# Kernel tuning notes

Measured on AMD Instinct MI355X. Metric: run time of the kernel, lower is better.

Reference implementation:

```python
import jax, jax.numpy as jnp
import numpy as np

N_NODES = 50000
N_EDGES = 312500
WIDTH = 256
LN_EPS = 1e-5


def setup_inputs() -> dict:
    key = jax.random.key(0)
    k1, k2, k3, k4 = jax.random.split(key, 4)
    x = jax.random.normal(k1, (N_NODES, WIDTH), dtype=jnp.float32)
    edge_index = jax.random.randint(k2, (2, N_EDGES), 0, N_NODES, dtype=jnp.int64)
    # GCNConv linear weight (out, in) and bias, LayerNorm affine params
    W = jax.random.normal(k3, (WIDTH, WIDTH), dtype=jnp.float32) / np.sqrt(WIDTH)
    b = jax.random.normal(k4, (WIDTH,), dtype=jnp.float32) * 0.01
    gamma = jnp.ones((WIDTH,), dtype=jnp.float32)
    beta = jnp.zeros((WIDTH,), dtype=jnp.float32)
    return {"x": x, "edge_index": edge_index, "W": W, "b": b, "gamma": gamma, "beta": beta}


def gcn_conv(x, edge_index, W, b):
    """PyG GCNConv: add self-loops, symmetric normalization, scatter-add aggregate."""
    n = x.shape[0]
    loops = jnp.arange(n, dtype=edge_index.dtype)
    src = jnp.concatenate([edge_index[0], loops])  # message source
    dst = jnp.concatenate([edge_index[1], loops])  # message destination
    # degree computed on destination nodes (including self-loops)
    deg = jax.ops.segment_sum(jnp.ones_like(dst, dtype=x.dtype), dst, num_segments=n)
    dinv = jnp.where(deg > 0, jax.lax.rsqrt(deg), 0.0)
    norm = dinv[src] * dinv[dst]  # [E+N]
    h = x @ W.T  # [N, width]
    msgs = norm[:, None] * h[src]  # [E+N, width]
    out = jax.ops.segment_sum(msgs, dst, num_segments=n)
    return out + b


def layer_norm(x, gamma, beta):
    mu = jnp.mean(x, axis=-1, keepdims=True)
    var = jnp.mean(jnp.square(x - mu), axis=-1, keepdims=True)
    return (x - mu) * jax.lax.rsqrt(var + LN_EPS) * gamma + beta


def reference(x, edge_index, W, b, gamma, beta):
    h = gcn_conv(x, edge_index, W, b)
    h = layer_norm(h, gamma, beta)
    h = jax.nn.relu(h)
    # dropout is identity in eval mode
    return h
```

## Files before the change

### kernel.cpp

```cpp
#include <hip/hip_runtime.h>
#include <hip/hip_bf16.h>

#define N_NODES 50000
#define N_EDGES 312500
#define WIDTH   256
#define LN_EPS  1e-5f
#define CAP     64

typedef __attribute__((ext_vector_type(8))) short bf16x8;
typedef __attribute__((ext_vector_type(4))) float f32x4;

__device__ __forceinline__ float bf_lo(unsigned u) { return __uint_as_float(u << 16); }
__device__ __forceinline__ float bf_hi(unsigned u) { return __uint_as_float(u & 0xffff0000u); }

__device__ __forceinline__ bf16x8 cvt8(float4 a, float4 b) {
    union { __hip_bfloat16 hh[8]; bf16x8 v; } u;
    u.hh[0] = __float2bfloat16(a.x); u.hh[1] = __float2bfloat16(a.y);
    u.hh[2] = __float2bfloat16(a.z); u.hh[3] = __float2bfloat16(a.w);
    u.hh[4] = __float2bfloat16(b.x); u.hh[5] = __float2bfloat16(b.y);
    u.hh[6] = __float2bfloat16(b.z); u.hh[7] = __float2bfloat16(b.w);
    return u.v;
}

__global__ __launch_bounds__(256) void gemm_mfma(const float* __restrict__ x,
                                                 const float* __restrict__ W,
                                                 __hip_bfloat16* __restrict__ h,
                                                 int* __restrict__ cnt) {
    if (blockIdx.y == 0) {
        int gid = blockIdx.x * 256 + threadIdx.x;
        if (gid < N_NODES) cnt[gid] = 0;
    }

    __shared__ short As[64][72];
    __shared__ short Bs[128][72];
    const int t    = threadIdx.x;
    const int lane = t & 63;
    const int wv   = t >> 6;
    const int wm   = wv & 1;
    const int wn   = wv >> 1;
    const int lrow = lane & 15;
    const int quad = lane >> 4;
    const int mrow0 = blockIdx.x * 64;
    const int ncol0 = blockIdx.y * 128;

    f32x4 acc[2][4];
    #pragma unroll
    for (int i = 0; i < 2; i++)
        #pragma unroll
        for (int j = 0; j < 4; j++)
            #pragma unroll
            for (int r = 0; r < 4; r++) acc[i][j][r] = 0.0f;

    const int sr = t >> 3;
    const int sg = t & 7;

    float4 pa0[2], pa1[2], pb0[4], pb1[4];
    auto load_chunk = [&](int k0) {
        #pragma unroll
        for (int p = 0; p < 2; p++) {
            int r  = p * 32 + sr;
            int gr = min(mrow0 + r, N_NODES - 1);
            const float* xp = x + (size_t)gr * WIDTH + k0 + sg * 8;
            pa0[p] = *(const float4*)xp;
            pa1[p] = *(const float4*)(xp + 4);
        }
        #pragma unroll
        for (int p = 0; p < 4; p++) {
            int gn = ncol0 + p * 32 + sr;
            const float* wp = W + (size_t)gn * WIDTH + k0 + sg * 8;
            pb0[p] = *(const float4*)wp;
            pb1[p] = *(const float4*)(wp + 4);
        }
    };

    load_chunk(0);
    for (int kc = 0; kc < 4; kc++) {
        if (kc) __syncthreads();
        #pragma unroll
        for (int p = 0; p < 2; p++)
            *(bf16x8*)&As[p * 32 + sr][sg * 8] = cvt8(pa0[p], pa1[p]);
        #pragma unroll
        for (int p = 0; p < 4; p++)
            *(bf16x8*)&Bs[p * 32 + sr][sg * 8] = cvt8(pb0[p], pb1[p]);
        __syncthreads();
        if (kc < 3) load_chunk((kc + 1) * 64);

        #pragma unroll
        for (int s = 0; s < 2; s++) {
            bf16x8 af[2], bfr[4];
            #pragma unroll
            for (int i = 0; i < 2; i++)
                af[i] = *(const bf16x8*)&As[wm * 32 + i * 16 + lrow][s * 32 + quad * 8];
            #pragma unroll
            for (int j = 0; j < 4; j++)
                bfr[j] = *(const bf16x8*)&Bs[wn * 64 + j * 16 + lrow][s * 32 + quad * 8];
            #pragma unroll
            for (int i = 0; i < 2; i++)
                #pragma unroll
                for (int j = 0; j < 4; j++)
                    acc[i][j] = __builtin_amdgcn_mfma_f32_16x16x32_bf16(
                        af[i], bfr[j], acc[i][j], 0, 0, 0);
        }
    }

    #pragma unroll
    for (int i = 0; i < 2; i++) {
        #pragma unroll
        for (int j = 0; j < 4; j++) {
            int col = ncol0 + wn * 64 + j * 16 + lrow;
            #pragma unroll
            for (int r = 0; r < 4; r++) {
                int gr = mrow0 + wm * 32 + i * 16 + quad * 4 + r;
                if (gr < N_NODES)
                    h[(size_t)gr * WIDTH + col] = __float2bfloat16(acc[i][j][r]);
            }
        }
    }
}

__global__ void fill_bucket(const int* __restrict__ src, const int* __restrict__ dst,
                            int* __restrict__ cnt, int* __restrict__ bucket, int e) {
    int i = blockIdx.x * blockDim.x + threadIdx.x;
    if (i < e) {
        int d = dst[i];
        int pos = atomicAdd(&cnt[d], 1);
        bucket[d * CAP + min(pos, CAP - 1)] = src[i];
    }
}

__global__ __launch_bounds__(256) void gather_ln(const __hip_bfloat16* __restrict__ h,
                                                 const int* __restrict__ cnt,
                                                 const int* __restrict__ bucket,
                                                 const float* __restrict__ b,
                                                 const float* __restrict__ gamma,
                                                 const float* __restrict__ beta,
                                                 float* __restrict__ out) {
    const int lane = threadIdx.x & 63;
    const int d    = blockIdx.x * 4 + (threadIdx.x >> 6);

    const uint2* hrows = (const uint2*)h;
    const int cd = min(cnt[d], CAP);
    const float dv = rsqrtf((float)(cd + 1));

    int   s  = 0;
    float sv = 0.0f;
    if (lane < cd) {
        s  = bucket[d * CAP + lane];
        sv = rsqrtf((float)(min(cnt[s], CAP) + 1));
    }

    uint2 hv = hrows[(size_t)d * 64 + lane];
    float a0 = dv * bf_lo(hv.x), a1 = dv * bf_hi(hv.x);
    float a2 = dv * bf_lo(hv.y), a3 = dv * bf_hi(hv.y);

    for (int q = 0; q < cd; q += 8) {
        int   si[8]; float wi[8]; uint2 ri[8];
        #pragma unroll
        for (int u = 0; u < 8; u++) {
            si[u] = __shfl(s, q + u, 64);
            wi[u] = __shfl(sv, q + u, 64);
        }
        #pragma unroll
        for (int u = 0; u < 8; u++)
            ri[u] = hrows[(size_t)si[u] * 64 + lane];
        #pragma unroll
        for (int u = 0; u < 8; u++) {
            a0 += wi[u] * bf_lo(ri[u].x); a1 += wi[u] * bf_hi(ri[u].x);
            a2 += wi[u] * bf_lo(ri[u].y); a3 += wi[u] * bf_hi(ri[u].y);
        }
    }

    float4 bv = *(const float4*)(b + lane * 4);
    float v0 = bv.x + dv * a0;
    float v1 = bv.y + dv * a1;
    float v2 = bv.z + dv * a2;
    float v3 = bv.w + dv * a3;

    float s1 = v0 + v1 + v2 + v3;
    float s2 = v0 * v0 + v1 * v1 + v2 * v2 + v3 * v3;
    #pragma unroll
    for (int off = 32; off > 0; off >>= 1) {
        s1 += __shfl_xor(s1, off, 64);
        s2 += __shfl_xor(s2, off, 64);
    }
    float mu   = s1 * (1.0f / 256.0f);
    float var  = s2 * (1.0f / 256.0f) - mu * mu;
    float rstd = rsqrtf(var + LN_EPS);

    float4 gv = *(const float4*)(gamma + lane * 4);
    float4 bt = *(const float4*)(beta + lane * 4);
    float4 y;
    y.x = fmaxf((v0 - mu) * rstd * gv.x + bt.x, 0.0f);
    y.y = fmaxf((v1 - mu) * rstd * gv.y + bt.y, 0.0f);
    y.z = fmaxf((v2 - mu) * rstd * gv.z + bt.z, 0.0f);
    y.w = fmaxf((v3 - mu) * rstd * gv.w + bt.w, 0.0f);
    *(float4*)(out + (size_t)d * WIDTH + lane * 4) = y;
}

extern "C" void kernel_launch(void* const* d_in, const int* in_sizes, int n_in,
                              void* d_out, int out_size, void* d_ws, size_t ws_size,
                              hipStream_t stream) {
    const float* x     = (const float*)d_in[0];
    const int*   ei    = (const int*)d_in[1];
    const float* W     = (const float*)d_in[2];
    const float* b     = (const float*)d_in[3];
    const float* gamma = (const float*)d_in[4];
    const float* beta  = (const float*)d_in[5];
    float* out = (float*)d_out;

    const int* src = ei;
    const int* dst = ei + N_EDGES;

    float* wsf = (float*)d_ws;
    __hip_bfloat16* h      = (__hip_bfloat16*)wsf;
    int*            cnt    = (int*)(wsf + 6400000);
    int*            bucket = (int*)(wsf + 6450048);

    dim3 ggrid((N_NODES + 63) / 64, 2);
    gemm_mfma<<<ggrid, 256, 0, stream>>>(x, W, h, cnt);

    fill_bucket<<<(N_EDGES + 255) / 256, 256, 0, stream>>>(src, dst, cnt, bucket, N_EDGES);

    gather_ln<<<N_NODES / 4, 256, 0, stream>>>(h, cnt, bucket, b, gamma, beta, out);
}
```

Baseline: 174.1 us.

## Fuse GEMM and bucket fill into one launch; use uniform neighbor loads in gather

```diff
diff --git a/kernel.cpp b/kernel.cpp
--- a/kernel.cpp
+++ b/kernel.cpp
@@ -6,6 +6,8 @@
 #define WIDTH   256
 #define LN_EPS  1e-5f
 #define CAP     64
+#define GEMM_BLKS 1564
+#define FILL_BLKS 1221
 
 typedef __attribute__((ext_vector_type(8))) short bf16x8;
 typedef __attribute__((ext_vector_type(4))) float f32x4;
@@ -22,13 +24,22 @@
     return u.v;
 }
 
-__global__ __launch_bounds__(256) void gemm_mfma(const float* __restrict__ x,
+__global__ __launch_bounds__(256) void gemm_fill(const float* __restrict__ x,
                                                  const float* __restrict__ W,
                                                  __hip_bfloat16* __restrict__ h,
-                                                 int* __restrict__ cnt) {
-    if (blockIdx.y == 0) {
-        int gid = blockIdx.x * 256 + threadIdx.x;
-        if (gid < N_NODES) cnt[gid] = 0;
+                                                 const int* __restrict__ src,
+                                                 const int* __restrict__ dst,
+                                                 int* __restrict__ cnt,
+                                                 int* __restrict__ bucket) {
+    const int blk = blockIdx.x;
+    if (blk >= GEMM_BLKS) {
+        int i = (blk - GEMM_BLKS) * 256 + threadIdx.x;
+        if (i < N_EDGES) {
+            int d = dst[i];
+            int pos = atomicAdd(&cnt[d], 1);
+            bucket[d * CAP + min(pos, CAP - 1)] = src[i];
+        }
+        return;
     }
 
     __shared__ short As[64][72];
@@ -40,8 +51,8 @@
     const int wn   = wv >> 1;
     const int lrow = lane & 15;
     const int quad = lane >> 4;
-    const int mrow0 = blockIdx.x * 64;
-    const int ncol0 = blockIdx.y * 128;
+    const int mrow0 = (blk >> 1) * 64;
+    const int ncol0 = (blk & 1) * 128;
 
     f32x4 acc[2][4];
     #pragma unroll
@@ -115,16 +126,6 @@
                     h[(size_t)gr * WIDTH + col] = __float2bfloat16(acc[i][j][r]);
             }
         }
-    }
-}
-
-__global__ void fill_bucket(const int* __restrict__ src, const int* __restrict__ dst,
-                            int* __restrict__ cnt, int* __restrict__ bucket, int e) {
-    int i = blockIdx.x * blockDim.x + threadIdx.x;
-    if (i < e) {
-        int d = dst[i];
-        int pos = atomicAdd(&cnt[d], 1);
-        bucket[d * CAP + min(pos, CAP - 1)] = src[i];
     }
 }
 
@@ -137,36 +138,35 @@
                                                  float* __restrict__ out) {
     const int lane = threadIdx.x & 63;
     const int d    = blockIdx.x * 4 + (threadIdx.x >> 6);
+    const int du   = __builtin_amdgcn_readfirstlane(d);
 
     const uint2* hrows = (const uint2*)h;
-    const int cd = min(cnt[d], CAP);
+    const int cd = min(cnt[du], CAP);
     const float dv = rsqrtf((float)(cd + 1));
-
-    int   s  = 0;
-    float sv = 0.0f;
-    if (lane < cd) {
-        s  = bucket[d * CAP + lane];
-        sv = rsqrtf((float)(min(cnt[s], CAP) + 1));
-    }
+    const int base = du * CAP;
 
     uint2 hv = hrows[(size_t)d * 64 + lane];
     float a0 = dv * bf_lo(hv.x), a1 = dv * bf_hi(hv.x);
     float a2 = dv * bf_lo(hv.y), a3 = dv * bf_hi(hv.y);
 
     for (int q = 0; q < cd; q += 8) {
-        int   si[8]; float wi[8]; uint2 ri[8];
+        int   sq[8]; float wq[8]; uint2 ri[8];
         #pragma unroll
         for (int u = 0; u < 8; u++) {
-            si[u] = __shfl(s, q + u, 64);
-            wi[u] = __shfl(sv, q + u, 64);
+            int idx = q + u;
+            int s = bucket[base + idx];
+            s = (idx < cd) ? s : 0;
+            sq[u] = s;
+            int cs = cnt[s];
+            wq[u] = (idx < cd) ? rsqrtf((float)(cs + 1)) : 0.0f;
         }
         #pragma unroll
         for (int u = 0; u < 8; u++)
-            ri[u] = hrows[(size_t)si[u] * 64 + lane];
+            ri[u] = hrows[(size_t)sq[u] * 64 + lane];
         #pragma unroll
         for (int u = 0; u < 8; u++) {
-            a0 += wi[u] * bf_lo(ri[u].x); a1 += wi[u] * bf_hi(ri[u].x);
-            a2 += wi[u] * bf_lo(ri[u].y); a3 += wi[u] * bf_hi(ri[u].y);
+            a0 += wq[u] * bf_lo(ri[u].x); a1 += wq[u] * bf_hi(ri[u].x);
+            a2 += wq[u] * bf_lo(ri[u].y); a3 += wq[u] * bf_hi(ri[u].y);
         }
     }
 
@@ -216,10 +216,9 @@
     int*            cnt    = (int*)(wsf + 6400000);
     int*            bucket = (int*)(wsf + 6450048);
 
-    dim3 ggrid((N_NODES + 63) / 64, 2);
-    gemm_mfma<<<ggrid, 256, 0, stream>>>(x, W, h, cnt);
-
-    fill_bucket<<<(N_EDGES + 255) / 256, 256, 0, stream>>>(src, dst, cnt, bucket, N_EDGES);
+    hipMemsetAsync(cnt, 0, N_NODES * sizeof(int), stream);
+
+    gemm_fill<<<GEMM_BLKS + FILL_BLKS, 256, 0, stream>>>(x, W, h, src, dst, cnt, bucket);
 
     gather_ln<<<N_NODES / 4, 256, 0, stream>>>(h, cnt, bucket, b, gamma, beta, out);
 }
```

Result: faster. 169.7 us (-2.5%).
